# Kernel optimization log

Hardware: AMD Instinct MI355X
Metric: run time of the kernel (lower is better)

The kernel has to match this reference:

```python
import jax, jax.numpy as jnp
import numpy as np

N = 262144  # points per batch (~4096 rays x 64 samples)
FDIM = 64   # plane feature dim
S = 512     # base plane resolution


def setup_inputs() -> dict:
    key = jax.random.key(0)
    ks = jax.random.split(key, 10)
    x = jax.random.uniform(ks[0], (N, 3), dtype=jnp.float32, minval=-1.0, maxval=1.0)
    rays_o = jnp.array([[0.0, 0.0, 1.5]], dtype=jnp.float32)  # ray origin; distances straddle 1.5/2.0
    scale = jnp.ones((3,), dtype=jnp.float32)
    plane = lambda k, s: jax.random.normal(k, (FDIM, s, s), dtype=jnp.float32)
    return {
        'x': x, 'rays_o': rays_o, 'scale': scale,
        'xy_plane': plane(ks[1], S), 'yz_plane': plane(ks[2], S), 'xz_plane': plane(ks[3], S),
        'xy_plane1': plane(ks[4], S // 2), 'yz_plane1': plane(ks[5], S // 2), 'xz_plane1': plane(ks[6], S // 2),
        'xy_plane2': plane(ks[7], S // 4), 'yz_plane2': plane(ks[8], S // 4), 'xz_plane2': plane(ks[9], S // 4),
    }


def bilinear_sample(plane, coords):
    """F.grid_sample(mode='bilinear', align_corners=True, padding_mode='zeros').
    plane: [C, H, W]; coords: [N, 2] with (x, y) in [-1, 1] (x indexes W).
    Returns [N, C]."""
    C, H, W = plane.shape
    fx = (coords[:, 0] + 1.0) * 0.5 * (W - 1)
    fy = (coords[:, 1] + 1.0) * 0.5 * (H - 1)
    x0 = jnp.floor(fx)
    y0 = jnp.floor(fy)
    wx = fx - x0
    wy = fy - y0
    x0i = x0.astype(jnp.int32)
    y0i = y0.astype(jnp.int32)

    def gather(xi, yi):
        valid = (xi >= 0) & (xi < W) & (yi >= 0) & (yi < H)
        xc = jnp.clip(xi, 0, W - 1)
        yc = jnp.clip(yi, 0, H - 1)
        v = plane[:, yc, xc]  # [C, N]
        return jnp.where(valid[None, :], v, 0.0)

    v00 = gather(x0i, y0i)
    v01 = gather(x0i + 1, y0i)
    v10 = gather(x0i, y0i + 1)
    v11 = gather(x0i + 1, y0i + 1)
    out = (v00 * (1 - wx) * (1 - wy) + v01 * wx * (1 - wy)
           + v10 * (1 - wx) * wy + v11 * wx * wy)  # [C, N]
    return out.T


def forward(x, rays_o, scale, xy0, yz0, xz0, xy1, yz1, xz1, xy2, yz2, xz2):
    xs = x * scale[None, :]
    xy_c = xs[:, :2]                                   # (x, y)
    xz_c = jnp.stack([xs[:, 0], xs[:, 2]], axis=-1)    # (x, z)
    yz_c = xs[:, 1:]                                   # (y, z)

    # laplace breakpoints: first index with distance > 1.5 / > 2.0 from rays_o[0]
    d = jnp.linalg.norm(rays_o[0][None, :] - xs, axis=-1)
    c1 = d > 1.5
    c2 = d > 2.0
    break1 = jnp.where(c1.any(), jnp.argmax(c1), 0)
    break2 = jnp.where(c2.any(), jnp.argmax(c2), 0)
    idx = jnp.arange(x.shape[0])
    # level 0: [0, break1), level 1: [break1, break2), level 2: [break2, N)
    level = jnp.where(idx < break1, 0, jnp.where(idx < break2, 1, 2))[:, None]

    def tri(p0, p1, p2, c):
        s0 = bilinear_sample(p0, c)
        s1 = bilinear_sample(p1, c)
        s2 = bilinear_sample(p2, c)
        # laplace: level1 = fine + half, level2 = fine + half + quarter
        return jnp.where(level == 0, s0, jnp.where(level == 1, s0 + s1, s0 + s1 + s2))

    return (tri(xy0, xy1, xy2, xy_c)
            + tri(xz0, xz1, xz2, xz_c)
            + tri(yz0, yz1, yz2, yz_c))


def reference(x, rays_o, scale, xy_plane, yz_plane, xz_plane, xy_plane1, yz_plane1, xz_plane1, xy_plane2, yz_plane2, xz_plane2):
    return forward(x, rays_o, scale, xy_plane, yz_plane, xz_plane,
                   xy_plane1, yz_plane1, xz_plane1,
                   xy_plane2, yz_plane2, xz_plane2)
```

## Files before the change

### kernel.cpp

```cpp
#include <hip/hip_runtime.h>
#include <hip/hip_fp16.h>

#define NPTS 262144
#define FDIM 64

__global__ __launch_bounds__(256) void break_kernel(const float* __restrict__ x,
                                                    const float* __restrict__ rays_o,
                                                    const float* __restrict__ scale,
                                                    unsigned* __restrict__ breaks) {
  const unsigned t = blockIdx.x * 256u + threadIdx.x;
  const float r0 = rays_o[0], r1 = rays_o[1], r2 = rays_o[2];
  const float s0 = scale[0], s1 = scale[1], s2 = scale[2];
  unsigned b1 = 0xFFFFFFFFu, b2 = 0xFFFFFFFFu;
  for (unsigned p = t; p < NPTS; p += 65536u) {
    const float dx = r0 - x[p * 3 + 0] * s0;
    const float dy = r1 - x[p * 3 + 1] * s1;
    const float dz = r2 - x[p * 3 + 2] * s2;
    const float d = sqrtf(__fadd_rn(__fadd_rn(__fmul_rn(dx, dx), __fmul_rn(dy, dy)),
                                    __fmul_rn(dz, dz)));
    if (d > 1.5f) b1 = min(b1, p);
    if (d > 2.0f) b2 = min(b2, p);
  }
  __shared__ unsigned sb1[256];
  __shared__ unsigned sb2[256];
  sb1[threadIdx.x] = b1;
  sb2[threadIdx.x] = b2;
  __syncthreads();
  for (int s = 128; s > 0; s >>= 1) {
    if ((int)threadIdx.x < s) {
      sb1[threadIdx.x] = min(sb1[threadIdx.x], sb1[threadIdx.x + s]);
      sb2[threadIdx.x] = min(sb2[threadIdx.x], sb2[threadIdx.x + s]);
    }
    __syncthreads();
  }
  if (threadIdx.x == 0) {
    atomicMin(&breaks[0], sb1[0]);
    atomicMin(&breaks[1], sb2[0]);
  }
}

__global__ __launch_bounds__(256) void transpose_kernel(const float* __restrict__ src,
                                                        __half* __restrict__ dst, int S) {
  __shared__ __half lds[64 * 66];
  const int t = threadIdx.x;
  const size_t SS = (size_t)S * S;
  const size_t p0 = (size_t)blockIdx.x * 64;
#pragma unroll
  for (int it = 0; it < 16; ++it) {
    const int c = it * 4 + (t >> 6);
    const int px = t & 63;
    const float v = src[(size_t)c * SS + p0 + px];
    lds[px * 66 + c] = __float2half(v);
  }
  __syncthreads();
#pragma unroll
  for (int it = 0; it < 16; ++it) {
    const int px = it * 4 + (t >> 6);
    const int c = t & 63;
    dst[(p0 + px) * FDIM + c] = lds[px * 66 + c];
  }
}

union H8 { uint4 u; __half h[8]; };

__device__ __forceinline__ void bilinear_weights(int W, float cx, float cy,
                                                 float& w00, float& w01, float& w10, float& w11,
                                                 int& xc0, int& xc1, int& yc0, int& yc1) {
  const float Wm1 = (float)(W - 1);
  const float fx = (cx + 1.0f) * 0.5f * Wm1;
  const float fy = (cy + 1.0f) * 0.5f * Wm1;
  const float x0f = floorf(fx), y0f = floorf(fy);
  const float wx = fx - x0f, wy = fy - y0f;
  const int ix = (int)x0f, iy = (int)y0f;
  const int ix1 = ix + 1, iy1 = iy + 1;
  const bool vx0 = (ix >= 0) && (ix < W);
  const bool vx1 = (ix1 >= 0) && (ix1 < W);
  const bool vy0 = (iy >= 0) && (iy < W);
  const bool vy1 = (iy1 >= 0) && (iy1 < W);
  xc0 = min(max(ix, 0), W - 1);
  xc1 = min(max(ix1, 0), W - 1);
  yc0 = min(max(iy, 0), W - 1);
  yc1 = min(max(iy1, 0), W - 1);
  w00 = (1.0f - wx) * (1.0f - wy) * (float)(vx0 && vy0);
  w01 = wx * (1.0f - wy) * (float)(vx1 && vy0);
  w10 = (1.0f - wx) * wy * (float)(vx0 && vy1);
  w11 = wx * wy * (float)(vx1 && vy1);
}

__device__ __forceinline__ void sample8_t(const __half* __restrict__ pl, int W,
                                          float cx, float cy, int j8, float acc[8]) {
  float w00, w01, w10, w11;
  int xc0, xc1, yc0, yc1;
  bilinear_weights(W, cx, cy, w00, w01, w10, w11, xc0, xc1, yc0, yc1);
  const __half* b00 = pl + ((size_t)(yc0 * W + xc0) * FDIM + j8);
  const __half* b01 = pl + ((size_t)(yc0 * W + xc1) * FDIM + j8);
  const __half* b10 = pl + ((size_t)(yc1 * W + xc0) * FDIM + j8);
  const __half* b11 = pl + ((size_t)(yc1 * W + xc1) * FDIM + j8);
  H8 v00, v01, v10, v11;
  v00.u = *(const uint4*)b00;
  v01.u = *(const uint4*)b01;
  v10.u = *(const uint4*)b10;
  v11.u = *(const uint4*)b11;
#pragma unroll
  for (int k = 0; k < 8; ++k) {
    acc[k] += w00 * __half2float(v00.h[k]) + w01 * __half2float(v01.h[k]) +
              w10 * __half2float(v10.h[k]) + w11 * __half2float(v11.h[k]);
  }
}

__device__ __forceinline__ void sample8_d(const float* __restrict__ pl, int W,
                                          float cx, float cy, int j8, float acc[8]) {
  float w00, w01, w10, w11;
  int xc0, xc1, yc0, yc1;
  bilinear_weights(W, cx, cy, w00, w01, w10, w11, xc0, xc1, yc0, yc1);
  const size_t SS = (size_t)W * W;
  const int i00 = yc0 * W + xc0, i01 = yc0 * W + xc1;
  const int i10 = yc1 * W + xc0, i11 = yc1 * W + xc1;
#pragma unroll
  for (int k = 0; k < 8; ++k) {
    const size_t co = (size_t)(j8 + k) * SS;
    acc[k] += w00 * pl[co + i00] + w01 * pl[co + i01] +
              w10 * pl[co + i10] + w11 * pl[co + i11];
  }
}

struct PlanesH { const __half* p[9]; };
struct PlanesF { const float* p[9]; };

__global__ __launch_bounds__(256) void sample_kernel(const float* __restrict__ x,
                                                     const float* __restrict__ scale,
                                                     const unsigned* __restrict__ breaks,
                                                     PlanesH tp, float* __restrict__ out) {
  const int t = blockIdx.x * 256 + threadIdx.x;
  const int p = t >> 3;
  const int j8 = (t & 7) * 8;
  const float s0 = scale[0], s1 = scale[1], s2 = scale[2];
  const float xs0 = x[p * 3 + 0] * s0;
  const float xs1 = x[p * 3 + 1] * s1;
  const float xs2 = x[p * 3 + 2] * s2;
  unsigned b1 = breaks[0]; if (b1 >= NPTS) b1 = 0;
  unsigned b2 = breaks[1]; if (b2 >= NPTS) b2 = 0;
  const unsigned pu = (unsigned)p;
  const int level = (pu < b1) ? 0 : ((pu < b2) ? 1 : 2);
  float acc[8];
#pragma unroll
  for (int k = 0; k < 8; ++k) acc[k] = 0.0f;
  sample8_t(tp.p[0], 512, xs0, xs1, j8, acc);
  sample8_t(tp.p[1], 512, xs1, xs2, j8, acc);
  sample8_t(tp.p[2], 512, xs0, xs2, j8, acc);
  if (level >= 1) {
    sample8_t(tp.p[3], 256, xs0, xs1, j8, acc);
    sample8_t(tp.p[4], 256, xs1, xs2, j8, acc);
    sample8_t(tp.p[5], 256, xs0, xs2, j8, acc);
  }
  if (level >= 2) {
    sample8_t(tp.p[6], 128, xs0, xs1, j8, acc);
    sample8_t(tp.p[7], 128, xs1, xs2, j8, acc);
    sample8_t(tp.p[8], 128, xs0, xs2, j8, acc);
  }
  float4* o4 = (float4*)(out + (size_t)p * FDIM + j8);
  o4[0] = make_float4(acc[0], acc[1], acc[2], acc[3]);
  o4[1] = make_float4(acc[4], acc[5], acc[6], acc[7]);
}

__global__ __launch_bounds__(256) void sample_kernel_direct(const float* __restrict__ x,
                                                            const float* __restrict__ scale,
                                                            const unsigned* __restrict__ breaks,
                                                            PlanesF tp, float* __restrict__ out) {
  const int t = blockIdx.x * 256 + threadIdx.x;
  const int p = t >> 3;
  const int j8 = (t & 7) * 8;
  const float s0 = scale[0], s1 = scale[1], s2 = scale[2];
  const float xs0 = x[p * 3 + 0] * s0;
  const float xs1 = x[p * 3 + 1] * s1;
  const float xs2 = x[p * 3 + 2] * s2;
  unsigned b1 = breaks[0]; if (b1 >= NPTS) b1 = 0;
  unsigned b2 = breaks[1]; if (b2 >= NPTS) b2 = 0;
  const unsigned pu = (unsigned)p;
  const int level = (pu < b1) ? 0 : ((pu < b2) ? 1 : 2);
  float acc[8];
#pragma unroll
  for (int k = 0; k < 8; ++k) acc[k] = 0.0f;
  sample8_d(tp.p[0], 512, xs0, xs1, j8, acc);
  sample8_d(tp.p[1], 512, xs1, xs2, j8, acc);
  sample8_d(tp.p[2], 512, xs0, xs2, j8, acc);
  if (level >= 1) {
    sample8_d(tp.p[3], 256, xs0, xs1, j8, acc);
    sample8_d(tp.p[4], 256, xs1, xs2, j8, acc);
    sample8_d(tp.p[5], 256, xs0, xs2, j8, acc);
  }
  if (level >= 2) {
    sample8_d(tp.p[6], 128, xs0, xs1, j8, acc);
    sample8_d(tp.p[7], 128, xs1, xs2, j8, acc);
    sample8_d(tp.p[8], 128, xs0, xs2, j8, acc);
  }
  float4* o4 = (float4*)(out + (size_t)p * FDIM + j8);
  o4[0] = make_float4(acc[0], acc[1], acc[2], acc[3]);
  o4[1] = make_float4(acc[4], acc[5], acc[6], acc[7]);
}

extern "C" void kernel_launch(void* const* d_in, const int* in_sizes, int n_in,
                              void* d_out, int out_size, void* d_ws, size_t ws_size,
                              hipStream_t stream) {
  const float* x = (const float*)d_in[0];
  const float* rays_o = (const float*)d_in[1];
  const float* scale = (const float*)d_in[2];
  const float* pl32[9];
  for (int i = 0; i < 9; ++i) pl32[i] = (const float*)d_in[3 + i];
  float* out = (float*)d_out;

  unsigned char* ws = (unsigned char*)d_ws;
  unsigned* breaks = (unsigned*)ws;

  hipMemsetAsync(d_ws, 0xFF, 8, stream);
  break_kernel<<<256, 256, 0, stream>>>(x, rays_o, scale, breaks);

  const int Ss[3] = {512, 256, 128};
  size_t need = 256;
  for (int l = 0; l < 3; ++l) need += 3 * (size_t)Ss[l] * Ss[l] * FDIM * sizeof(__half);

  if (ws_size >= need) {
    PlanesH tp;
    size_t off = 256;
    for (int l = 0; l < 3; ++l) {
      const int S = Ss[l];
      const int SS = S * S;
      for (int o = 0; o < 3; ++o) {
        __half* dst = (__half*)(ws + off);
        tp.p[l * 3 + o] = dst;
        transpose_kernel<<<SS / 64, 256, 0, stream>>>(pl32[l * 3 + o], dst, S);
        off += (size_t)SS * FDIM * sizeof(__half);
      }
    }
    sample_kernel<<<(NPTS * 8) / 256, 256, 0, stream>>>(x, scale, breaks, tp, out);
  } else {
    PlanesF tf;
    for (int i = 0; i < 9; ++i) tf.p[i] = pl32[i];
    sample_kernel_direct<<<(NPTS * 8) / 256, 256, 0, stream>>>(x, scale, breaks, tf, out);
  }
}
```

Baseline: 467.6 us.

## Merge nine plane transposes into one launch with vectorized loads/stores

Replaces nine separate transpose launches with one kernel that maps each block to a plane through a prefix table of tile counts. Global reads now use float4 and LDS-to-global writes use 16-byte stores, cutting the number of memory instructions. The sample kernel's output writes become nontemporal stores so they do not pollute cache. The aim is less launch overhead and better bandwidth use in the transpose prologue, which re-reads about 150MB of fp32 planes on every call. In exchange, each block does a small lookup to find its plane, and the strided 2-byte LDS writes may cause bank conflicts.

```diff
diff --git a/kernel.cpp b/kernel.cpp
--- a/kernel.cpp
+++ b/kernel.cpp
@@ -3,6 +3,8 @@
 
 #define NPTS 262144
 #define FDIM 64
+
+typedef float vfloat4 __attribute__((ext_vector_type(4)));
 
 __global__ __launch_bounds__(256) void break_kernel(const float* __restrict__ x,
                                                     const float* __restrict__ rays_o,
@@ -39,25 +41,49 @@
   }
 }
 
-__global__ __launch_bounds__(256) void transpose_kernel(const float* __restrict__ src,
-                                                        __half* __restrict__ dst, int S) {
+struct TransposeArgs {
+  const float* src[9];
+  __half* dst[9];
+  int tile_hi[9];
+  int SS[9];
+};
+
+__global__ __launch_bounds__(256) void transpose_all(TransposeArgs a) {
   __shared__ __half lds[64 * 66];
+  const int tile = blockIdx.x;
+  int pi = 0;
+#pragma unroll
+  for (int i = 0; i < 9; ++i) {
+    if (tile >= a.tile_hi[i]) pi = i + 1;
+  }
+  const int lo = (pi == 0) ? 0 : a.tile_hi[pi - 1];
+  const float* __restrict__ src = a.src[pi];
+  __half* __restrict__ dst = a.dst[pi];
+  const size_t SS = (size_t)a.SS[pi];
+  const size_t p0 = (size_t)(tile - lo) * 64;
+
   const int t = threadIdx.x;
-  const size_t SS = (size_t)S * S;
-  const size_t p0 = (size_t)blockIdx.x * 64;
-#pragma unroll
-  for (int it = 0; it < 16; ++it) {
-    const int c = it * 4 + (t >> 6);
-    const int px = t & 63;
-    const float v = src[(size_t)c * SS + p0 + px];
-    lds[px * 66 + c] = __float2half(v);
+  const int px4 = t & 15;
+  const int cg = t >> 4;
+#pragma unroll
+  for (int it = 0; it < 4; ++it) {
+    const int c = it * 16 + cg;
+    const float4 v = *(const float4*)(src + (size_t)c * SS + p0 + (size_t)px4 * 4);
+    lds[(px4 * 4 + 0) * 66 + c] = __float2half(v.x);
+    lds[(px4 * 4 + 1) * 66 + c] = __float2half(v.y);
+    lds[(px4 * 4 + 2) * 66 + c] = __float2half(v.z);
+    lds[(px4 * 4 + 3) * 66 + c] = __float2half(v.w);
   }
   __syncthreads();
-#pragma unroll
-  for (int it = 0; it < 16; ++it) {
-    const int px = it * 4 + (t >> 6);
-    const int c = t & 63;
-    dst[(p0 + px) * FDIM + c] = lds[px * 66 + c];
+  const int c8 = t & 7;
+  const int pxo = t >> 3;
+#pragma unroll
+  for (int it = 0; it < 2; ++it) {
+    const int px = it * 32 + pxo;
+    const unsigned* w = (const unsigned*)(lds + px * 66 + c8 * 8);
+    uint4 v;
+    v.x = w[0]; v.y = w[1]; v.z = w[2]; v.w = w[3];
+    *(uint4*)(dst + (p0 + (size_t)px) * FDIM + c8 * 8) = v;
   }
 }
 
@@ -158,9 +184,11 @@
     sample8_t(tp.p[7], 128, xs1, xs2, j8, acc);
     sample8_t(tp.p[8], 128, xs0, xs2, j8, acc);
   }
-  float4* o4 = (float4*)(out + (size_t)p * FDIM + j8);
-  o4[0] = make_float4(acc[0], acc[1], acc[2], acc[3]);
-  o4[1] = make_float4(acc[4], acc[5], acc[6], acc[7]);
+  float* o = out + (size_t)p * FDIM + j8;
+  vfloat4 lo = {acc[0], acc[1], acc[2], acc[3]};
+  vfloat4 hi = {acc[4], acc[5], acc[6], acc[7]};
+  __builtin_nontemporal_store(lo, (vfloat4*)o);
+  __builtin_nontemporal_store(hi, (vfloat4*)(o + 4));
 }
 
 __global__ __launch_bounds__(256) void sample_kernel_direct(const float* __restrict__ x,
@@ -212,7 +240,7 @@
   unsigned char* ws = (unsigned char*)d_ws;
   unsigned* breaks = (unsigned*)ws;
 
-  hipMemsetAsync(d_ws, 0xFF, 8, stream);
+  (void)hipMemsetAsync(d_ws, 0xFF, 8, stream);
   break_kernel<<<256, 256, 0, stream>>>(x, rays_o, scale, breaks);
 
   const int Ss[3] = {512, 256, 128};
@@ -221,17 +249,25 @@
 
   if (ws_size >= need) {
     PlanesH tp;
+    TransposeArgs ta;
     size_t off = 256;
+    int tiles_acc = 0;
     for (int l = 0; l < 3; ++l) {
       const int S = Ss[l];
       const int SS = S * S;
       for (int o = 0; o < 3; ++o) {
+        const int i = l * 3 + o;
         __half* dst = (__half*)(ws + off);
-        tp.p[l * 3 + o] = dst;
-        transpose_kernel<<<SS / 64, 256, 0, stream>>>(pl32[l * 3 + o], dst, S);
+        tp.p[i] = dst;
+        ta.src[i] = pl32[i];
+        ta.dst[i] = dst;
+        ta.SS[i] = SS;
+        tiles_acc += SS / 64;
+        ta.tile_hi[i] = tiles_acc;
         off += (size_t)SS * FDIM * sizeof(__half);
       }
     }
+    transpose_all<<<tiles_acc, 256, 0, stream>>>(ta);
     sample_kernel<<<(NPTS * 8) / 256, 256, 0, stream>>>(x, scale, breaks, tp, out);
   } else {
     PlanesF tf;
```

Result: faster. 446.2 us (-4.6%).
